# Performance work log

Hardware: AMD Instinct MI355X
Metric: run time of the kernel (lower is better)

Reference implementation:

```python
import jax, jax.numpy as jnp
import numpy as np

B, S, HID = 2, 2048, 2048
H, D, KV = 16, 128, 4          # heads, head_dim, kv heads
REP = H // KV                  # GQA repeat factor
THETA = 10000.0


def setup_inputs() -> dict:
    key = jax.random.key(0)
    ks = jax.random.split(key, 12)
    query = jax.random.normal(ks[0], (B, S, HID), jnp.float32)
    k_in = jax.random.normal(ks[1], (B, S, HID), jnp.float32)
    v_in = jax.random.normal(ks[2], (B, S, HID), jnp.float32)
    # additive causal mask: 0 on/below diag, -10000 above
    causal = jnp.tril(jnp.ones((S, S), jnp.float32))
    mask = jnp.broadcast_to((1.0 - causal) * -10000.0, (B, 1, S, S))
    # rotary tables (cos/sin of freqs_cis), shape [S, D//2]
    inv_freq = 1.0 / (THETA ** (jnp.arange(0, D, 2, dtype=jnp.float32) / D))
    ang = jnp.outer(jnp.arange(S, dtype=jnp.float32), inv_freq)
    freqs_cos, freqs_sin = jnp.cos(ang), jnp.sin(ang)
    sd = 0.02
    Wq = jax.random.normal(ks[3], (HID, H * D), jnp.float32) * sd
    bq = jnp.zeros((H * D,), jnp.float32)
    Wk = jax.random.normal(ks[4], (HID, KV * D), jnp.float32) * sd
    bk = jnp.zeros((KV * D,), jnp.float32)
    Wv = jax.random.normal(ks[5], (HID, KV * D), jnp.float32) * sd
    bv = jnp.zeros((KV * D,), jnp.float32)
    Wo = jax.random.normal(ks[6], (H * D, HID), jnp.float32) * sd
    bo = jnp.zeros((HID,), jnp.float32)
    return {"query": query, "key": k_in, "value": v_in, "mask": mask,
            "freqs_cos": freqs_cos, "freqs_sin": freqs_sin,
            "Wq": Wq, "bq": bq, "Wk": Wk, "bk": bk,
            "Wv": Wv, "bv": bv, "Wo": Wo, "bo": bo}


def _rope(x, cos, sin):
    # x: [B,S,h,D]; pairs adjacent dims as complex (view_as_complex)
    xr = x.reshape(*x.shape[:-1], D // 2, 2)
    xe, xo = xr[..., 0], xr[..., 1]
    c = cos[None, :, None, :]
    s = sin[None, :, None, :]
    re = xe * c - xo * s
    im = xe * s + xo * c
    return jnp.stack([re, im], axis=-1).reshape(x.shape)


def reference(query, key, value, mask, freqs_cos, freqs_sin,
              Wq, bq, Wk, bk, Wv, bv, Wo, bo):
    q = (query @ Wq + bq).reshape(B, S, H, D)
    k = (key @ Wk + bk).reshape(B, S, KV, D)
    v = (value @ Wv + bv).reshape(B, S, KV, D)
    # repeat_kv: torch.repeat_interleave along head dim
    k = jnp.repeat(k, REP, axis=2)
    v = jnpp_repeat = jnp.repeat(v, REP, axis=2)
    q = _rope(q, freqs_cos, freqs_sin)
    k = _rope(k, freqs_cos, freqs_sin)
    q = q.transpose(0, 2, 1, 3)  # [B,H,S,D]
    k = k.transpose(0, 2, 1, 3)
    v = v.transpose(0, 2, 1, 3)
    scores = jnp.einsum('bhqd,bhkd->bhqk', q, k) / jnp.sqrt(jnp.float32(D))
    scores = scores + mask
    probs = jax.nn.softmax(scores, axis=-1)
    ctx = jnp.einsum('bhqk,bhkd->bhqd', probs, v)
    ctx = ctx.transpose(0, 2, 1, 3).reshape(B, S, H * D)
    return ctx @ Wo + bo
```

## Files before the change

### kernel.cpp

```cpp
#include <hip/hip_runtime.h>
#include <stdint.h>

#define BB 2
#define SS 2048
#define HID 2048
#define NH 16
#define DD 128
#define NKV 4

typedef unsigned short u16;
typedef __attribute__((ext_vector_type(8))) short short8;
typedef __attribute__((ext_vector_type(4))) float f32x4;

#if __has_builtin(__builtin_amdgcn_exp2f)
#define EXP2(x) __builtin_amdgcn_exp2f(x)
#else
#define EXP2(x) exp2f(x)
#endif

__device__ __forceinline__ u16 f2bf(float x) {
    union { float f; unsigned u; } v; v.f = x;
    unsigned u = v.u;
    return (u16)((u + 0x7FFFu + ((u >> 16) & 1u)) >> 16);
}

__device__ __forceinline__ void async_lds16(const void* g, void* l) {
    __builtin_amdgcn_global_load_lds(
        (const __attribute__((address_space(1))) void*)(uintptr_t)g,
        (__attribute__((address_space(3))) void*)(uintptr_t)l,
        16, 0, 0);
}

__global__ __launch_bounds__(256) void k_prep(const float* __restrict__ query,
                                              const float* __restrict__ key,
                                              const float* __restrict__ value,
                                              const float* __restrict__ Wq,
                                              const float* __restrict__ Wk,
                                              const float* __restrict__ Wv,
                                              const float* __restrict__ Wo,
                                              u16* __restrict__ qbf,
                                              u16* __restrict__ kbf,
                                              u16* __restrict__ vbf,
                                              u16* __restrict__ Wt,
                                              u16* __restrict__ Wot) {
    __shared__ float tile[32][33];
    int x = blockIdx.x;
    if (x < 24576) {
        const float* in; u16* out;
        if (x < 8192)       { in = query; out = qbf; }
        else if (x < 16384) { in = key;   out = kbf; x -= 8192; }
        else                { in = value; out = vbf; x -= 16384; }
        const int i = x * 256 + threadIdx.x;
        float4 v = ((const float4*)in)[i];
        uint2 o;
        o.x = (unsigned)f2bf(v.x) | ((unsigned)f2bf(v.y) << 16);
        o.y = (unsigned)f2bf(v.z) | ((unsigned)f2bf(v.w) << 16);
        ((uint2*)out)[i] = o;
        return;
    }
    const int v_ = x - 24576;
    const int ty = v_ / 160;
    const int xt = v_ - ty * 160;
    const float* src; u16* dst; int N, n0;
    if (xt < 64)      { src = Wq; dst = Wt;                          N = 2048; n0 = xt * 32; }
    else if (xt < 80) { src = Wk; dst = Wt + (size_t)2048 * 2048;    N = 512;  n0 = (xt - 64) * 32; }
    else if (xt < 96) { src = Wv; dst = Wt + (size_t)2560 * 2048;    N = 512;  n0 = (xt - 80) * 32; }
    else              { src = Wo; dst = Wot;                         N = 2048; n0 = (xt - 96) * 32; }
    const int k0 = ty * 32;
    const int c = threadIdx.x & 31, r = threadIdx.x >> 5;
#pragma unroll
    for (int i = 0; i < 32; i += 8)
        tile[r + i][c] = src[(size_t)(k0 + r + i) * N + n0 + c];
    __syncthreads();
#pragma unroll
    for (int i = 0; i < 32; i += 8)
        dst[(size_t)(n0 + r + i) * 2048 + k0 + c] = f2bf(tile[c][r + i]);
}

__device__ __forceinline__ void gemm256_loop(const u16* __restrict__ gA,
                                             const u16* __restrict__ gB,
                                             const int K, char* smem,
                                             const int wave, const int lane,
                                             f32x4 (&acc)[8][4]) {
    const int r = lane & 15, q4 = lane >> 4;
    const int wr = wave >> 2, wc = wave & 3;
    u16* As = (u16*)smem;
    u16* Bs = (u16*)(smem + 65536);

    int aoff[8], boff[4];
#pragma unroll
    for (int i = 0; i < 8; i++) {
        const int ar = wr * 128 + i * 16 + r;
        aoff[i] = ar * 64 + ((q4 ^ (ar & 7)) << 3);
    }
#pragma unroll
    for (int j = 0; j < 4; j++) {
        const int br = wc * 64 + j * 16 + r;
        boff[j] = br * 64 + ((q4 ^ (br & 7)) << 3);
    }

    const int nt = K >> 6;

#define STG_A(buf, i, T) async_lds16(gA + (size_t)(i) * 64 * K + (size_t)(T) * 64, \
                                     smem + (buf) * 32768 + ((i) * 64 + wave * 8) * 128)
#define STG_B(buf, i, T) async_lds16(gB + (size_t)(i) * 64 * K + (size_t)(T) * 64, \
                                     smem + 65536 + (buf) * 32768 + ((i) * 64 + wave * 8) * 128)

    STG_A(0, 0, 0); STG_A(0, 1, 0); STG_A(0, 2, 0); STG_A(0, 3, 0);
    STG_B(0, 0, 0); STG_B(0, 1, 0); STG_B(0, 2, 0); STG_B(0, 3, 0);
    STG_B(1, 0, 1); STG_B(1, 1, 1); STG_B(1, 2, 1); STG_B(1, 3, 1);
    asm volatile("s_waitcnt vmcnt(4)" ::: "memory");
    __builtin_amdgcn_s_barrier();

    short8 Af[4][2], Bf[4][2];
    for (int t = 0; t < nt; t++) {
        const int cur = t & 1;
        const u16* Ab = As + cur * 16384;
        const u16* Bb = Bs + cur * 16384;
        const bool p1v = (t + 1 < nt);
        const bool p2v = (t + 2 < nt);

#pragma unroll
        for (int i = 0; i < 4; i++) {
            Af[i][0] = *(const short8*)(Ab + aoff[i]);
            Af[i][1] = *(const short8*)(Ab + (aoff[i] ^ 32));
        }
#pragma unroll
        for (int j = 0; j < 2; j++) {
            Bf[j][0] = *(const short8*)(Bb + boff[j]);
            Bf[j][1] = *(const short8*)(Bb + (boff[j] ^ 32));
        }
        if (p1v) { STG_A(cur ^ 1, 0, t + 1); STG_A(cur ^ 1, 1, t + 1); }
        __builtin_amdgcn_s_barrier();
        asm volatile("s_waitcnt lgkmcnt(0)" ::: "memory");
        __builtin_amdgcn_s_setprio(1);
#pragma unroll
        for (int kk = 0; kk < 2; kk++)
#pragma unroll
            for (int i = 0; i < 4; i++)
#pragma unroll
                for (int j = 0; j < 2; j++)
                    acc[i][j] = __builtin_amdgcn_mfma_f32_16x16x32_bf16(Af[i][kk], Bf[j][kk], acc[i][j], 0, 0, 0);
        __builtin_amdgcn_s_setprio(0);
        __builtin_amdgcn_s_barrier();

#pragma unroll
        for (int j = 2; j < 4; j++) {
            Bf[j][0] = *(const short8*)(Bb + boff[j]);
            Bf[j][1] = *(const short8*)(Bb + (boff[j] ^ 32));
        }
        if (p1v) { STG_A(cur ^ 1, 2, t + 1); STG_A(cur ^ 1, 3, t + 1); }
        __builtin_amdgcn_s_barrier();
        asm volatile("s_waitcnt lgkmcnt(0)" ::: "memory");
        __builtin_amdgcn_s_setprio(1);
#pragma unroll
        for (int kk = 0; kk < 2; kk++)
#pragma unroll
            for (int i = 0; i < 4; i++)
#pragma unroll
                for (int j = 2; j < 4; j++)
                    acc[i][j] = __builtin_amdgcn_mfma_f32_16x16x32_bf16(Af[i][kk], Bf[j][kk], acc[i][j], 0, 0, 0);
        __builtin_amdgcn_s_setprio(0);
        __builtin_amdgcn_s_barrier();

#pragma unroll
        for (int i = 0; i < 4; i++) {
            Af[i][0] = *(const short8*)(Ab + aoff[i + 4]);
            Af[i][1] = *(const short8*)(Ab + (aoff[i + 4] ^ 32));
        }
        if (p2v) { STG_B(cur, 0, t + 2); STG_B(cur, 1, t + 2); }
        __builtin_amdgcn_s_barrier();
        asm volatile("s_waitcnt lgkmcnt(0)" ::: "memory");
        __builtin_amdgcn_s_setprio(1);
#pragma unroll
        for (int kk = 0; kk < 2; kk++)
#pragma unroll
            for (int i = 0; i < 4; i++)
#pragma unroll
                for (int j = 2; j < 4; j++)
                    acc[i + 4][j] = __builtin_amdgcn_mfma_f32_16x16x32_bf16(Af[i][kk], Bf[j][kk], acc[i + 4][j], 0, 0, 0);
        __builtin_amdgcn_s_setprio(0);
        __builtin_amdgcn_s_barrier();

        if (p2v) {
            STG_B(cur, 2, t + 2); STG_B(cur, 3, t + 2);
            asm volatile("s_waitcnt vmcnt(4)" ::: "memory");
        } else {
            asm volatile("s_waitcnt vmcnt(0)" ::: "memory");
        }
        __builtin_amdgcn_s_barrier();
        __builtin_amdgcn_s_setprio(1);
#pragma unroll
        for (int kk = 0; kk < 2; kk++)
#pragma unroll
            for (int i = 0; i < 4; i++)
#pragma unroll
                for (int j = 0; j < 2; j++)
                    acc[i + 4][j] = __builtin_amdgcn_mfma_f32_16x16x32_bf16(Af[i][kk], Bf[j][kk], acc[i + 4][j], 0, 0, 0);
        __builtin_amdgcn_s_setprio(0);
        __builtin_amdgcn_s_barrier();
    }
#undef STG_A
#undef STG_B
}

__global__ __launch_bounds__(512, 2) void k_gemm_qkv(const u16* __restrict__ qbf,
                                                     const u16* __restrict__ kbf,
                                                     const u16* __restrict__ vbf,
                                                     const u16* __restrict__ Wt,
                                                     const float* __restrict__ bq,
                                                     const float* __restrict__ bk,
                                                     const float* __restrict__ bv,
                                                     const float* __restrict__ fc,
                                                     const float* __restrict__ fs,
                                                     u16* __restrict__ qro,
                                                     u16* __restrict__ kro,
                                                     u16* __restrict__ vtr) {
    __shared__ char smem[131072];
    const int tid = threadIdx.x;
    const int lane = tid & 63, wave = tid >> 6;
    const int wr = wave >> 2, wc = wave & 3;
    const int r = lane & 15, q4 = lane >> 4;

    const int bid0 = blockIdx.y * 12 + blockIdx.x;
    const int nb = (bid0 & 7) * 24 + (bid0 >> 3);
    const int bx = nb % 12;
    const int bm0 = (nb / 12) * 256;

    const u16* A = (bx < 8) ? qbf : (bx < 10) ? kbf : vbf;

    const int srow = wave * 8 + (lane >> 3);
    const int c0 = ((lane & 7) ^ (lane >> 3)) * 8;
    const u16* gA = A  + (size_t)(bm0 + srow) * 2048 + c0;
    const u16* gB = Wt + (size_t)(bx * 256 + srow) * 2048 + c0;

    f32x4 acc[8][4] = {};
    gemm256_loop(gA, gB, 2048, smem, wave, lane, acc);

    if (bx < 10) {
        const bool isQ = (bx < 8);
        const float qsc = isQ ? 0.08838834764831845f * 1.4426950408889634f : 1.0f;
        const float* bias = isQ ? bq : bk;
        u16* base = isQ ? qro : kro;
        const int nheads = isQ ? NH : NKV;

        float* ep = (float*)smem + wave * 2560;
#pragma unroll
        for (int j = 0; j < 4; j++) {
            const int gc = bx * 256 + wc * 64 + j * 16;
            const int head = isQ ? (gc >> 7) : ((gc - 2048) >> 7);
            const int d0 = gc & 127;
            const float bcol = bias[head * 128 + d0 + r];
#pragma unroll
            for (int i = 0; i < 8; i++)
#pragma unroll
                for (int g = 0; g < 4; g++)
                    ep[(i * 16 + q4 * 4 + g) * 20 + r] = acc[i][j][g] + bcol;
#pragma unroll
            for (int rr = 0; rr < 2; rr++) {
                const int row = rr * 64 + lane;
                const int grow = bm0 + wr * 128 + row;
                const int s = grow & 2047, bidx = grow >> 11;
                const float* fcp0 = fc + s * 64;
                const float* fsp0 = fs + s * 64;
                float4 x0 = *(float4*)(ep + row * 20 + 0);
                float4 x1 = *(float4*)(ep + row * 20 + 4);
                float4 x2 = *(float4*)(ep + row * 20 + 8);
                float4 x3 = *(float4*)(ep + row * 20 + 12);
                const int ii0 = d0 >> 1;
                float4 ca = *(const float4*)(fcp0 + ii0);
                float4 cb = *(const float4*)(fcp0 + ii0 + 4);
                float4 sa = *(const float4*)(fsp0 + ii0);
                float4 sb = *(const float4*)(fsp0 + ii0 + 4);
                float o[16];
                o[0]  = (x0.x * ca.x - x0.y * sa.x) * qsc;  o[1]  = (x0.x * sa.x + x0.y * ca.x) * qsc;
                o[2]  = (x0.z * ca.y - x0.w * sa.y) * qsc;  o[3]  = (x0.z * sa.y + x0.w * ca.y) * qsc;
                o[4]  = (x1.x * ca.z - x1.y * sa.z) * qsc;  o[5]  = (x1.x * sa.z + x1.y * ca.z) * qsc;
                o[6]  = (x1.z * ca.w - x1.w * sa.w) * qsc;  o[7]  = (x1.z * sa.w + x1.w * ca.w) * qsc;
                o[8]  = (x2.x * cb.x - x2.y * sb.x) * qsc;  o[9]  = (x2.x * sb.x + x2.y * cb.x) * qsc;
                o[10] = (x2.z * cb.y - x2.w * sb.y) * qsc;  o[11] = (x2.z * sb.y + x2.w * cb.y) * qsc;
                o[12] = (x3.x * cb.z - x3.y * sb.z) * qsc;  o[13] = (x3.x * sb.z + x3.y * cb.z) * qsc;
                o[14] = (x3.z * cb.w - x3.w * sb.w) * qsc;  o[15] = (x3.z * sb.w + x3.w * cb.w) * qsc;
                unsigned w0 = (unsigned)f2bf(o[0])  | ((unsigned)f2bf(o[1])  << 16);
                unsigned w1 = (unsigned)f2bf(o[2])  | ((unsigned)f2bf(o[3])  << 16);
                unsigned w2 = (unsigned)f2bf(o[4])  | ((unsigned)f2bf(o[5])  << 16);
                unsigned w3 = (unsigned)f2bf(o[6])  | ((unsigned)f2bf(o[7])  << 16);
                unsigned w4 = (unsigned)f2bf(o[8])  | ((unsigned)f2bf(o[9])  << 16);
                unsigned w5 = (unsigned)f2bf(o[10]) | ((unsigned)f2bf(o[11]) << 16);
                unsigned w6 = (unsigned)f2bf(o[12]) | ((unsigned)f2bf(o[13]) << 16);
                unsigned w7 = (unsigned)f2bf(o[14]) | ((unsigned)f2bf(o[15]) << 16);
                u16* dst = base + (((size_t)(bidx * nheads + head) * SS + s) << 7) + d0;
                *(uint4*)dst = make_uint4(w0, w1, w2, w3);
                *(uint4*)(dst + 8) = make_uint4(w4, w5, w6, w7);
            }
        }
    } else {
#pragma unroll
        for (int j = 0; j < 4; j++) {
            const int colb = bx * 256 + wc * 64 + j * 16 + r - 2560;
            const int d = colb & 127, kv = colb >> 7;
            const float bb = bv[colb];
#pragma unroll
            for (int i = 0; i < 8; i++) {
                const int row0 = bm0 + wr * 128 + i * 16 + q4 * 4;
                const int s0 = row0 & 2047, b = row0 >> 11;
                uint2 o;
                o.x = (unsigned)f2bf(acc[i][j][0] + bb) | ((unsigned)f2bf(acc[i][j][1] + bb) << 16);
                o.y = (unsigned)f2bf(acc[i][j][2] + bb) | ((unsigned)f2bf(acc[i][j][3] + bb) << 16);
                *(uint2*)(vtr + ((size_t)(b * NKV + kv) * DD + d) * SS + s0) = o;
            }
        }
    }
}

__global__ __launch_bounds__(512, 2) void k_gemm_bt(const u16* __restrict__ A,
                                                    const u16* __restrict__ Bt,
                                                    const float* __restrict__ bias,
                                                    float* __restrict__ C,
                                                    int M, int N, int K) {
    __shared__ char smem[131072];
    const int tid = threadIdx.x;
    const int lane = tid & 63, wave = tid >> 6;
    const int wr = wave >> 2, wc = wave & 3;
    const int r = lane & 15, q4 = lane >> 4;

    const int bid0 = blockIdx.y * 8 + blockIdx.x;
    const int nb = (bid0 & 7) * 16 + (bid0 >> 3);
    const int bn0 = (nb % 8) * 256;
    const int bm0 = (nb / 8) * 256;

    const int srow = wave * 8 + (lane >> 3);
    const int c0 = ((lane & 7) ^ (lane >> 3)) * 8;
    const u16* gA = A  + (size_t)(bm0 + srow) * K + c0;
    const u16* gB = Bt + (size_t)(bn0 + srow) * K + c0;

    f32x4 acc[8][4] = {};
    gemm256_loop(gA, gB, K, smem, wave, lane, acc);

#pragma unroll
    for (int j = 0; j < 4; j++) {
        const int col = bn0 + wc * 64 + j * 16 + r;
        const float bb = bias[col];
#pragma unroll
        for (int i = 0; i < 8; i++) {
            const int row = bm0 + wr * 128 + i * 16 + q4 * 4;
#pragma unroll
            for (int g = 0; g < 4; g++)
                C[(size_t)(row + g) * N + col] = acc[i][j][g] + bb;
        }
    }
}

__global__ __launch_bounds__(256) void k_attn(const u16* __restrict__ Q,
                                              const u16* __restrict__ K_,
                                              const u16* __restrict__ V_,
                                              u16* __restrict__ Ctx) {
    __shared__ u16 Ks[3][32 * 128];
    __shared__ u16 Vs[3][128 * 32];
    __shared__ u16 Pb[4][32 * 48];

    const int tid = threadIdx.x;
    const int lane = tid & 63, wave = tid >> 6;
    const int bh = blockIdx.x;
    const int b = bh >> 4, h = bh & 15;
    const int kvh = (b << 2) | (h >> 2);
    const int qb = (gridDim.y - 1 - blockIdx.y) * 128;
    const int qcol = lane & 15, q4 = lane >> 4;
    const int qw = qb + wave * 32;

    const u16* Qg = Q + ((size_t)bh * SS + qw + qcol) * DD;
    short8 qfr[2][4];
#pragma unroll
    for (int qi = 0; qi < 2; qi++)
#pragma unroll
        for (int c = 0; c < 4; c++)
            qfr[qi][c] = *(const short8*)(Qg + qi * 16 * DD + c * 32 + q4 * 8);

    const u16* Kg = K_ + (size_t)kvh * SS * DD;
    const u16* Vg = V_ + (size_t)kvh * DD * SS;

    const int krow = tid >> 4;
    const int kchunk = (tid & 15) ^ (krow & 7);
    const int vd = tid >> 2;
    const int vchunk = (tid & 3) ^ ((vd >> 1) & 3);

    const int nt = (qb + 128) >> 5;
    const int kmax = (nt - 1) * 32;

    f32x4 lacc[2] = {};
    f32x4 oacc[2][8] = {};

    const short8 ones = {0x3F80, 0x3F80, 0x3F80, 0x3F80, 0x3F80, 0x3F80, 0x3F80, 0x3F80};
    u16* pb = &Pb[wave][0];
    unsigned* pb32 = (unsigned*)pb;

#define STAGE_KV(T, BUF) do {                                                            \
        const int kb_ = min((T) * 32, kmax);                                             \
        async_lds16(Kg + (size_t)(kb_ + krow) * DD + kchunk * 8,      &Ks[BUF][0] + wave * 512); \
        async_lds16(Kg + (size_t)(kb_ + 16 + krow) * DD + kchunk * 8, &Ks[BUF][0] + 2048 + wave * 512); \
        async_lds16(Vg + (size_t)vd * SS + kb_ + vchunk * 8,          &Vs[BUF][0] + wave * 512); \
        async_lds16(Vg + (size_t)(vd + 64) * SS + kb_ + vchunk * 8,   &Vs[BUF][0] + 2048 + wave * 512); \
    } while (0)

    STAGE_KV(0, 0);
    STAGE_KV(1, 1);
    asm volatile("s_waitcnt vmcnt(4)\n\ts_barrier" ::: "memory");

    for (int t = 0; t < nt; t++) {
        const int kb = t * 32;
        const int cur = t % 3;
        STAGE_KV(t + 2, (t + 2) % 3);
        const u16* Ksc = &Ks[cur][0];
        const u16* Vsc = &Vs[cur][0];

        if (kb <= qw + 31) {
            f32x4 sc[2][2] = {};
            __builtin_amdgcn_s_setprio(1);
#pragma unroll
            for (int kt = 0; kt < 2; kt++) {
                const int kr = kt * 16 + qcol;
#pragma unroll
                for (int c = 0; c < 4; c++) {
                    short8 kf = *(const short8*)(Ksc + kr * 128 + (((c * 4 + q4) ^ (kr & 7)) << 3));
                    sc[kt][0] = __builtin_amdgcn_mfma_f32_16x16x32_bf16(kf, qfr[0][c], sc[kt][0], 0, 0, 0);
                    sc[kt][1] = __builtin_amdgcn_mfma_f32_16x16x32_bf16(kf, qfr[1][c], sc[kt][1], 0, 0, 0);
                }
            }
            __builtin_amdgcn_s_setprio(0);

            if (kb + 32 > qw) {
#pragma unroll
                for (int kt = 0; kt < 2; kt++)
#pragma unroll
                    for (int qi = 0; qi < 2; qi++)
#pragma unroll
                        for (int g = 0; g < 4; g++) {
                            const int key = kb + kt * 16 + q4 * 4 + g;
                            if (key > qw + qi * 16 + qcol) sc[kt][qi][g] = -1e30f;
                        }
            }

            const unsigned sel = 0x07060302u;
#pragma unroll
            for (int qi = 0; qi < 2; qi++) {
                float p0 = EXP2(sc[0][qi][0]), p1 = EXP2(sc[0][qi][1]);
                float p2 = EXP2(sc[0][qi][2]), p3 = EXP2(sc[0][qi][3]);
                float p4 = EXP2(sc[1][qi][0]), p5 = EXP2(sc[1][qi][1]);
                float p6 = EXP2(sc[1][qi][2]), p7 = EXP2(sc[1][qi][3]);
                unsigned pk0 = __builtin_amdgcn_perm(__float_as_uint(p1), __float_as_uint(p0), sel);
                unsigned pk1 = __builtin_amdgcn_perm(__float_as_uint(p3), __float_as_uint(p2), sel);
                unsigned pk2 = __builtin_amdgcn_perm(__float_as_uint(p5), __float_as_uint(p4), sel);
                unsigned pk3 = __builtin_amdgcn_perm(__float_as_uint(p7), __float_as_uint(p6), sel);
                const int row = qi * 16 + qcol;
                *(uint2*)(pb32 + row * 24 + 2 * q4)     = make_uint2(pk0, pk1);
                *(uint2*)(pb32 + row * 24 + 8 + 2 * q4) = make_uint2(pk2, pk3);
            }

            short8 pf0 = *(const short8*)(pb + qcol * 48 + q4 * 8);
            short8 pf1 = *(const short8*)(pb + (16 + qcol) * 48 + q4 * 8);

            __builtin_amdgcn_s_setprio(1);
            lacc[0] = __builtin_amdgcn_mfma_f32_16x16x32_bf16(ones, pf0, lacc[0], 0, 0, 0);
            lacc[1] = __builtin_amdgcn_mfma_f32_16x16x32_bf16(ones, pf1, lacc[1], 0, 0, 0);
#pragma unroll
            for (int dt = 0; dt < 8; dt++) {
                const int vr = dt * 16 + qcol;
                short8 vfr = *(const short8*)(Vsc + vr * 32 + ((q4 ^ ((vr >> 1) & 3)) << 3));
                oacc[0][dt] = __builtin_amdgcn_mfma_f32_16x16x32_bf16(vfr, pf0, oacc[0][dt], 0, 0, 0);
                oacc[1][dt] = __builtin_amdgcn_mfma_f32_16x16x32_bf16(vfr, pf1, oacc[1][dt], 0, 0, 0);
            }
            __builtin_amdgcn_s_setprio(0);
        }
        asm volatile("s_waitcnt vmcnt(4)\n\ts_barrier" ::: "memory");
    }
#undef STAGE_KV

#pragma unroll
    for (int qi = 0; qi < 2; qi++) {
        const float inv = 1.0f / lacc[qi][0];
        u16* outp = Ctx + ((size_t)b * SS + qw + qi * 16 + qcol) * (NH * DD) + h * DD;
#pragma unroll
        for (int dt = 0; dt < 8; dt++) {
            unsigned lo = (unsigned)f2bf(oacc[qi][dt][0] * inv) | ((unsigned)f2bf(oacc[qi][dt][1] * inv) << 16);
            unsigned hi = (unsigned)f2bf(oacc[qi][dt][2] * inv) | ((unsigned)f2bf(oacc[qi][dt][3] * inv) << 16);
            *(uint2*)(outp + dt * 16 + q4 * 4) = make_uint2(lo, hi);
        }
    }
}

extern "C" void kernel_launch(void* const* d_in, const int* in_sizes, int n_in,
                              void* d_out, int out_size, void* d_ws, size_t ws_size,
                              hipStream_t stream) {
    const float* query = (const float*)d_in[0];
    const float* key   = (const float*)d_in[1];
    const float* value = (const float*)d_in[2];
    const float* fc    = (const float*)d_in[4];
    const float* fs    = (const float*)d_in[5];
    const float* Wq    = (const float*)d_in[6];
    const float* bq    = (const float*)d_in[7];
    const float* Wk    = (const float*)d_in[8];
    const float* bk    = (const float*)d_in[9];
    const float* Wv    = (const float*)d_in[10];
    const float* bv    = (const float*)d_in[11];
    const float* Wo    = (const float*)d_in[12];
    const float* bo    = (const float*)d_in[13];
    float* out = (float*)d_out;

    char* w = (char*)d_ws;
    u16* qbf = (u16*)(w);
    u16* kbf = (u16*)(w + 16777216);
    u16* vbf = (u16*)(w + 33554432);
    u16* Wt  = (u16*)(w + 50331648);
    u16* Wot = (u16*)(w + 62914560);
    u16* qro = (u16*)(w + 71303168);
    u16* kro = (u16*)(w + 88080384);
    u16* vtr = (u16*)(w + 92274688);
    u16* ctx = (u16*)(w + 96468992);

    k_prep<<<34816, 256, 0, stream>>>(query, key, value, Wq, Wk, Wv, Wo,
                                      qbf, kbf, vbf, Wt, Wot);
    k_gemm_qkv<<<dim3(12, 16), 512, 0, stream>>>(qbf, kbf, vbf, Wt, bq, bk, bv,
                                                 fc, fs, qro, kro, vtr);
    k_attn<<<dim3(32, 16), 256, 0, stream>>>(qro, kro, vtr, ctx);
    k_gemm_bt<<<dim3(8, 16), 512, 0, stream>>>(ctx, Wot, bo, out, 4096, 2048, 2048);
}
```

Baseline: 404.3 us.

## Retile output GEMM to 256x128 blocks and double-buffer 64-key attention tiles

The output projection GEMM moves from 256x256 tiles (128 blocks) to 256x128 tiles (256 blocks) with a new inline double-buffered pipeline. Each wave holds a 64x64 accumulator, and the K loop is split into four MFMA phases with staggered async LDS loads. The attention kernel switches from triple-buffered 32-key stages to double-buffered 64-key stages, processed as two 32-key halves, and shrinks the P scratch padding. The aim is better CU occupancy and wave balance for the GEMM and fewer barriers in attention, at the cost of less prefetch depth in attention (a full vmcnt(0) wait each stage) and possible LDS bank conflicts from the new P stride.

```diff
diff --git a/kernel.cpp b/kernel.cpp
--- a/kernel.cpp
+++ b/kernel.cpp
@@ -318,32 +318,149 @@
                                                     const float* __restrict__ bias,
                                                     float* __restrict__ C,
                                                     int M, int N, int K) {
-    __shared__ char smem[131072];
+    __shared__ char smem[98304];
     const int tid = threadIdx.x;
     const int lane = tid & 63, wave = tid >> 6;
-    const int wr = wave >> 2, wc = wave & 3;
+    const int wr = wave >> 1, wc = wave & 1;
     const int r = lane & 15, q4 = lane >> 4;
 
-    const int bid0 = blockIdx.y * 8 + blockIdx.x;
-    const int nb = (bid0 & 7) * 16 + (bid0 >> 3);
-    const int bn0 = (nb % 8) * 256;
-    const int bm0 = (nb / 8) * 256;
+    const int bid0 = blockIdx.y * 16 + blockIdx.x;
+    const int nb = (bid0 & 7) * 32 + (bid0 >> 3);
+    const int bn0 = (nb & 15) * 128;
+    const int bm0 = (nb >> 4) * 256;
 
     const int srow = wave * 8 + (lane >> 3);
     const int c0 = ((lane & 7) ^ (lane >> 3)) * 8;
     const u16* gA = A  + (size_t)(bm0 + srow) * K + c0;
     const u16* gB = Bt + (size_t)(bn0 + srow) * K + c0;
 
-    f32x4 acc[8][4] = {};
-    gemm256_loop(gA, gB, K, smem, wave, lane, acc);
+    u16* As = (u16*)smem;
+    u16* Bs = (u16*)(smem + 65536);
+
+    int aoff[4], boff[4];
+#pragma unroll
+    for (int i = 0; i < 4; i++) {
+        const int ar = wr * 64 + i * 16 + r;
+        aoff[i] = ar * 64 + ((q4 ^ (ar & 7)) << 3);
+    }
+#pragma unroll
+    for (int j = 0; j < 4; j++) {
+        const int br = wc * 64 + j * 16 + r;
+        boff[j] = br * 64 + ((q4 ^ (br & 7)) << 3);
+    }
+
+    const int nt = K >> 6;
+
+#define STG_A(buf, i, T) async_lds16(gA + (size_t)(i) * 64 * K + (size_t)(T) * 64, \
+                                     smem + (buf) * 32768 + ((i) * 64 + wave * 8) * 128)
+#define STG_B(buf, i, T) async_lds16(gB + (size_t)(i) * 64 * K + (size_t)(T) * 64, \
+                                     smem + 65536 + (buf) * 16384 + ((i) * 64 + wave * 8) * 128)
+
+    STG_A(0, 0, 0); STG_A(0, 1, 0); STG_A(0, 2, 0); STG_A(0, 3, 0);
+    STG_B(0, 0, 0); STG_B(0, 1, 0);
+    STG_B(1, 0, 1); STG_B(1, 1, 1);
+    asm volatile("s_waitcnt vmcnt(2)" ::: "memory");
+    __builtin_amdgcn_s_barrier();
+
+    f32x4 acc[4][4] = {};
+    short8 Af[2][2], Bf[4][2];
+    for (int t = 0; t < nt; t++) {
+        const int cur = t & 1;
+        const u16* Ab = As + cur * 16384;
+        const u16* Bb = Bs + cur * 8192;
+        const bool p1v = (t + 1 < nt);
+        const bool p2v = (t + 2 < nt);
+
+#pragma unroll
+        for (int i = 0; i < 2; i++) {
+            Af[i][0] = *(const short8*)(Ab + aoff[i]);
+            Af[i][1] = *(const short8*)(Ab + (aoff[i] ^ 32));
+        }
+#pragma unroll
+        for (int j = 0; j < 2; j++) {
+            Bf[j][0] = *(const short8*)(Bb + boff[j]);
+            Bf[j][1] = *(const short8*)(Bb + (boff[j] ^ 32));
+        }
+        if (p1v) { STG_A(cur ^ 1, 0, t + 1); STG_A(cur ^ 1, 1, t + 1); }
+        __builtin_amdgcn_s_barrier();
+        asm volatile("s_waitcnt lgkmcnt(0)" ::: "memory");
+        __builtin_amdgcn_s_setprio(1);
+#pragma unroll
+        for (int kk = 0; kk < 2; kk++)
+#pragma unroll
+            for (int i = 0; i < 2; i++)
+#pragma unroll
+                for (int j = 0; j < 2; j++)
+                    acc[i][j] = __builtin_amdgcn_mfma_f32_16x16x32_bf16(Af[i][kk], Bf[j][kk], acc[i][j], 0, 0, 0);
+        __builtin_amdgcn_s_setprio(0);
+        __builtin_amdgcn_s_barrier();
+
+#pragma unroll
+        for (int j = 2; j < 4; j++) {
+            Bf[j][0] = *(const short8*)(Bb + boff[j]);
+            Bf[j][1] = *(const short8*)(Bb + (boff[j] ^ 32));
+        }
+        if (p1v) { STG_A(cur ^ 1, 2, t + 1); STG_A(cur ^ 1, 3, t + 1); }
+        __builtin_amdgcn_s_barrier();
+        asm volatile("s_waitcnt lgkmcnt(0)" ::: "memory");
+        __builtin_amdgcn_s_setprio(1);
+#pragma unroll
+        for (int kk = 0; kk < 2; kk++)
+#pragma unroll
+            for (int i = 0; i < 2; i++)
+#pragma unroll
+                for (int j = 2; j < 4; j++)
+                    acc[i][j] = __builtin_amdgcn_mfma_f32_16x16x32_bf16(Af[i][kk], Bf[j][kk], acc[i][j], 0, 0, 0);
+        __builtin_amdgcn_s_setprio(0);
+        __builtin_amdgcn_s_barrier();
+
+#pragma unroll
+        for (int i = 0; i < 2; i++) {
+            Af[i][0] = *(const short8*)(Ab + aoff[i + 2]);
+            Af[i][1] = *(const short8*)(Ab + (aoff[i + 2] ^ 32));
+        }
+        if (p2v) { STG_B(cur, 0, t + 2); }
+        __builtin_amdgcn_s_barrier();
+        asm volatile("s_waitcnt lgkmcnt(0)" ::: "memory");
+        __builtin_amdgcn_s_setprio(1);
+#pragma unroll
+        for (int kk = 0; kk < 2; kk++)
+#pragma unroll
+            for (int i = 0; i < 2; i++)
+#pragma unroll
+                for (int j = 2; j < 4; j++)
+                    acc[i + 2][j] = __builtin_amdgcn_mfma_f32_16x16x32_bf16(Af[i][kk], Bf[j][kk], acc[i + 2][j], 0, 0, 0);
+        __builtin_amdgcn_s_setprio(0);
+        __builtin_amdgcn_s_barrier();
+
+        if (p2v) {
+            STG_B(cur, 1, t + 2);
+            asm volatile("s_waitcnt vmcnt(2)" ::: "memory");
+        } else {
+            asm volatile("s_waitcnt vmcnt(0)" ::: "memory");
+        }
+        __builtin_amdgcn_s_barrier();
+        __builtin_amdgcn_s_setprio(1);
+#pragma unroll
+        for (int kk = 0; kk < 2; kk++)
+#pragma unroll
+            for (int i = 0; i < 2; i++)
+#pragma unroll
+                for (int j = 0; j < 2; j++)
+                    acc[i + 2][j] = __builtin_amdgcn_mfma_f32_16x16x32_bf16(Af[i][kk], Bf[j][kk], acc[i + 2][j], 0, 0, 0);
+        __builtin_amdgcn_s_setprio(0);
+        __builtin_amdgcn_s_barrier();
+    }
+#undef STG_A
+#undef STG_B
 
 #pragma unroll
     for (int j = 0; j < 4; j++) {
         const int col = bn0 + wc * 64 + j * 16 + r;
         const float bb = bias[col];
 #pragma unroll
-        for (int i = 0; i < 8; i++) {
-            const int row = bm0 + wr * 128 + i * 16 + q4 * 4;
+        for (int i = 0; i < 4; i++) {
+            const int row = bm0 + wr * 64 + i * 16 + q4 * 4;
 #pragma unroll
             for (int g = 0; g < 4; g++)
                 C[(size_t)(row + g) * N + col] = acc[i][j][g] + bb;
@@ -355,9 +472,9 @@
                                               const u16* __restrict__ K_,
                                               const u16* __restrict__ V_,
                                               u16* __restrict__ Ctx) {
-    __shared__ u16 Ks[3][32 * 128];
-    __shared__ u16 Vs[3][128 * 32];
-    __shared__ u16 Pb[4][32 * 48];
+    __shared__ u16 Ks[2][64 * 128];
+    __shared__ u16 Vs[2][2 * 128 * 32];
+    __shared__ u16 Pb[4][32 * 40];
 
     const int tid = threadIdx.x;
     const int lane = tid & 63, wave = tid >> 6;
@@ -384,8 +501,8 @@
     const int vd = tid >> 2;
     const int vchunk = (tid & 3) ^ ((vd >> 1) & 3);
 
-    const int nt = (qb + 128) >> 5;
-    const int kmax = (nt - 1) * 32;
+    const int nt = (qb + 128) >> 6;
+    const int kmax = (nt - 1) * 64;
 
     f32x4 lacc[2] = {};
     f32x4 oacc[2][8] = {};
@@ -394,84 +511,91 @@
     u16* pb = &Pb[wave][0];
     unsigned* pb32 = (unsigned*)pb;
 
-#define STAGE_KV(T, BUF) do {                                                            \
-        const int kb_ = min((T) * 32, kmax);                                             \
-        async_lds16(Kg + (size_t)(kb_ + krow) * DD + kchunk * 8,      &Ks[BUF][0] + wave * 512); \
-        async_lds16(Kg + (size_t)(kb_ + 16 + krow) * DD + kchunk * 8, &Ks[BUF][0] + 2048 + wave * 512); \
-        async_lds16(Vg + (size_t)vd * SS + kb_ + vchunk * 8,          &Vs[BUF][0] + wave * 512); \
-        async_lds16(Vg + (size_t)(vd + 64) * SS + kb_ + vchunk * 8,   &Vs[BUF][0] + 2048 + wave * 512); \
+#define STAGE_KV(T, BUF) do {                                                                   \
+        const int kb_ = min((T) * 64, kmax);                                                    \
+        async_lds16(Kg + (size_t)(kb_ + krow) * DD + kchunk * 8,        &Ks[BUF][0] + wave * 512);        \
+        async_lds16(Kg + (size_t)(kb_ + 16 + krow) * DD + kchunk * 8,   &Ks[BUF][0] + 2048 + wave * 512); \
+        async_lds16(Kg + (size_t)(kb_ + 32 + krow) * DD + kchunk * 8,   &Ks[BUF][0] + 4096 + wave * 512); \
+        async_lds16(Kg + (size_t)(kb_ + 48 + krow) * DD + kchunk * 8,   &Ks[BUF][0] + 6144 + wave * 512); \
+        async_lds16(Vg + (size_t)vd * SS + kb_ + vchunk * 8,            &Vs[BUF][0] + wave * 512);        \
+        async_lds16(Vg + (size_t)vd * SS + kb_ + 32 + vchunk * 8,       &Vs[BUF][0] + 4096 + wave * 512); \
+        async_lds16(Vg + (size_t)(vd + 64) * SS + kb_ + vchunk * 8,     &Vs[BUF][0] + 2048 + wave * 512); \
+        async_lds16(Vg + (size_t)(vd + 64) * SS + kb_ + 32 + vchunk * 8,&Vs[BUF][0] + 6144 + wave * 512); \
     } while (0)
 
     STAGE_KV(0, 0);
-    STAGE_KV(1, 1);
-    asm volatile("s_waitcnt vmcnt(4)\n\ts_barrier" ::: "memory");
 
     for (int t = 0; t < nt; t++) {
-        const int kb = t * 32;
-        const int cur = t % 3;
-        STAGE_KV(t + 2, (t + 2) % 3);
-        const u16* Ksc = &Ks[cur][0];
-        const u16* Vsc = &Vs[cur][0];
-
-        if (kb <= qw + 31) {
-            f32x4 sc[2][2] = {};
-            __builtin_amdgcn_s_setprio(1);
-#pragma unroll
-            for (int kt = 0; kt < 2; kt++) {
-                const int kr = kt * 16 + qcol;
-#pragma unroll
-                for (int c = 0; c < 4; c++) {
-                    short8 kf = *(const short8*)(Ksc + kr * 128 + (((c * 4 + q4) ^ (kr & 7)) << 3));
-                    sc[kt][0] = __builtin_amdgcn_mfma_f32_16x16x32_bf16(kf, qfr[0][c], sc[kt][0], 0, 0, 0);
-                    sc[kt][1] = __builtin_amdgcn_mfma_f32_16x16x32_bf16(kf, qfr[1][c], sc[kt][1], 0, 0, 0);
+        const int kb = t * 64;
+        const int cur = t & 1;
+        asm volatile("s_waitcnt vmcnt(0)\n\ts_barrier" ::: "memory");
+        if (t + 1 < nt) STAGE_KV(t + 1, cur ^ 1);
+
+#pragma unroll
+        for (int hh = 0; hh < 2; hh++) {
+            const int kbh = kb + hh * 32;
+            if (kbh <= qw + 31) {
+                const u16* Ksc = &Ks[cur][hh * 32 * 128];
+                const u16* Vsc = &Vs[cur][hh * 4096];
+
+                f32x4 sc[2][2] = {};
+                __builtin_amdgcn_s_setprio(1);
+#pragma unroll
+                for (int kt = 0; kt < 2; kt++) {
+                    const int kr = kt * 16 + qcol;
+#pragma unroll
+                    for (int c = 0; c < 4; c++) {
+                        short8 kf = *(const short8*)(Ksc + kr * 128 + (((c * 4 + q4) ^ (kr & 7)) << 3));
+                        sc[kt][0] = __builtin_amdgcn_mfma_f32_16x16x32_bf16(kf, qfr[0][c], sc[kt][0], 0, 0, 0);
+                        sc[kt][1] = __builtin_amdgcn_mfma_f32_16x16x32_bf16(kf, qfr[1][c], sc[kt][1], 0, 0, 0);
+                    }
                 }
+                __builtin_amdgcn_s_setprio(0);
+
+                if (kbh + 32 > qw) {
+#pragma unroll
+                    for (int kt = 0; kt < 2; kt++)
+#pragma unroll
+                        for (int qi = 0; qi < 2; qi++)
+#pragma unroll
+                            for (int g = 0; g < 4; g++) {
+                                const int key = kbh + kt * 16 + q4 * 4 + g;
+                                if (key > qw + qi * 16 + qcol) sc[kt][qi][g] = -1e30f;
+                            }
+                }
+
+                const unsigned sel = 0x07060302u;
+#pragma unroll
+                for (int qi = 0; qi < 2; qi++) {
+                    float p0 = EXP2(sc[0][qi][0]), p1 = EXP2(sc[0][qi][1]);
+                    float p2 = EXP2(sc[0][qi][2]), p3 = EXP2(sc[0][qi][3]);
+                    float p4 = EXP2(sc[1][qi][0]), p5 = EXP2(sc[1][qi][1]);
+                    float p6 = EXP2(sc[1][qi][2]), p7 = EXP2(sc[1][qi][3]);
+                    unsigned pk0 = __builtin_amdgcn_perm(__float_as_uint(p1), __float_as_uint(p0), sel);
+                    unsigned pk1 = __builtin_amdgcn_perm(__float_as_uint(p3), __float_as_uint(p2), sel);
+                    unsigned pk2 = __builtin_amdgcn_perm(__float_as_uint(p5), __float_as_uint(p4), sel);
+                    unsigned pk3 = __builtin_amdgcn_perm(__float_as_uint(p7), __float_as_uint(p6), sel);
+                    const int row = qi * 16 + qcol;
+                    *(uint2*)(pb32 + row * 20 + 2 * q4)     = make_uint2(pk0, pk1);
+                    *(uint2*)(pb32 + row * 20 + 8 + 2 * q4) = make_uint2(pk2, pk3);
+                }
+
+                short8 pf0 = *(const short8*)(pb + qcol * 40 + q4 * 8);
+                short8 pf1 = *(const short8*)(pb + (16 + qcol) * 40 + q4 * 8);
+
+                __builtin_amdgcn_s_setprio(1);
+                lacc[0] = __builtin_amdgcn_mfma_f32_16x16x32_bf16(ones, pf0, lacc[0], 0, 0, 0);
+                lacc[1] = __builtin_amdgcn_mfma_f32_16x16x32_bf16(ones, pf1, lacc[1], 0, 0, 0);
+#pragma unroll
+                for (int dt = 0; dt < 8; dt++) {
+                    const int vr = dt * 16 + qcol;
+                    short8 vfr = *(const short8*)(Vsc + vr * 32 + ((q4 ^ ((vr >> 1) & 3)) << 3));
+                    oacc[0][dt] = __builtin_amdgcn_mfma_f32_16x16x32_bf16(vfr, pf0, oacc[0][dt], 0, 0, 0);
+                    oacc[1][dt] = __builtin_amdgcn_mfma_f32_16x16x32_bf16(vfr, pf1, oacc[1][dt], 0, 0, 0);
+                }
+                __builtin_amdgcn_s_setprio(0);
             }
-            __builtin_amdgcn_s_setprio(0);
-
-            if (kb + 32 > qw) {
-#pragma unroll
-                for (int kt = 0; kt < 2; kt++)
-#pragma unroll
-                    for (int qi = 0; qi < 2; qi++)
-#pragma unroll
-                        for (int g = 0; g < 4; g++) {
-                            const int key = kb + kt * 16 + q4 * 4 + g;
-                            if (key > qw + qi * 16 + qcol) sc[kt][qi][g] = -1e30f;
-                        }
-            }
-
-            const unsigned sel = 0x07060302u;
-#pragma unroll
-            for (int qi = 0; qi < 2; qi++) {
-                float p0 = EXP2(sc[0][qi][0]), p1 = EXP2(sc[0][qi][1]);
-                float p2 = EXP2(sc[0][qi][2]), p3 = EXP2(sc[0][qi][3]);
-                float p4 = EXP2(sc[1][qi][0]), p5 = EXP2(sc[1][qi][1]);
-                float p6 = EXP2(sc[1][qi][2]), p7 = EXP2(sc[1][qi][3]);
-                unsigned pk0 = __builtin_amdgcn_perm(__float_as_uint(p1), __float_as_uint(p0), sel);
-                unsigned pk1 = __builtin_amdgcn_perm(__float_as_uint(p3), __float_as_uint(p2), sel);
-                unsigned pk2 = __builtin_amdgcn_perm(__float_as_uint(p5), __float_as_uint(p4), sel);
-                unsigned pk3 = __builtin_amdgcn_perm(__float_as_uint(p7), __float_as_uint(p6), sel);
-                const int row = qi * 16 + qcol;
-                *(uint2*)(pb32 + row * 24 + 2 * q4)     = make_uint2(pk0, pk1);
-                *(uint2*)(pb32 + row * 24 + 8 + 2 * q4) = make_uint2(pk2, pk3);
-            }
-
-            short8 pf0 = *(const short8*)(pb + qcol * 48 + q4 * 8);
-            short8 pf1 = *(const short8*)(pb + (16 + qcol) * 48 + q4 * 8);
-
-            __builtin_amdgcn_s_setprio(1);
-            lacc[0] = __builtin_amdgcn_mfma_f32_16x16x32_bf16(ones, pf0, lacc[0], 0, 0, 0);
-            lacc[1] = __builtin_amdgcn_mfma_f32_16x16x32_bf16(ones, pf1, lacc[1], 0, 0, 0);
-#pragma unroll
-            for (int dt = 0; dt < 8; dt++) {
-                const int vr = dt * 16 + qcol;
-                short8 vfr = *(const short8*)(Vsc + vr * 32 + ((q4 ^ ((vr >> 1) & 3)) << 3));
-                oacc[0][dt] = __builtin_amdgcn_mfma_f32_16x16x32_bf16(vfr, pf0, oacc[0][dt], 0, 0, 0);
-                oacc[1][dt] = __builtin_amdgcn_mfma_f32_16x16x32_bf16(vfr, pf1, oacc[1][dt], 0, 0, 0);
-            }
-            __builtin_amdgcn_s_setprio(0);
-        }
-        asm volatile("s_waitcnt vmcnt(4)\n\ts_barrier" ::: "memory");
+        }
     }
 #undef STAGE_KV
 
@@ -522,5 +646,5 @@
     k_gemm_qkv<<<dim3(12, 16), 512, 0, stream>>>(qbf, kbf, vbf, Wt, bq, bk, bv,
                                                  fc, fs, qro, kro, vtr);
     k_attn<<<dim3(32, 16), 256, 0, stream>>>(qro, kro, vtr, ctx);
-    k_gemm_bt<<<dim3(8, 16), 512, 0, stream>>>(ctx, Wot, bo, out, 4096, 2048, 2048);
-}
+    k_gemm_bt<<<dim3(16, 16), 512, 0, stream>>>(ctx, Wot, bo, out, 4096, 2048, 2048);
+}
```

New measurement: 366.0 us. 9.5% less time.
